# Performance work log

Hardware: AMD Instinct MI355X
Metric: run time of the kernel (lower is better)

## Reference

```python
import jax, jax.numpy as jnp
import numpy as np

N, E, G = 50000, 800000, 16
NODE, HID, OUT, HEADS = 128, 64, 128, 3
NEG_SLOPE = 0.2

def setup_inputs() -> dict:
    key = jax.random.key(0)
    ks = jax.random.split(key, 12)
    h = jax.random.normal(ks[0], (N, NODE), jnp.float32)
    z = jax.random.normal(ks[1], (G, OUT), jnp.float32)
    src = jax.random.randint(ks[2], (E,), 0, N, jnp.int32)
    dst = jax.random.randint(ks[3], (E,), 0, N, jnp.int32)
    graph_id = jnp.sort(jax.random.randint(ks[4], (N,), 0, G, jnp.int32))
    s = 0.1
    fc_w = jax.random.normal(ks[5], (HEADS * HID, NODE), jnp.float32) * s
    attn_l = jax.random.normal(ks[6], (HEADS, HID), jnp.float32) * s
    attn_r = jax.random.normal(ks[7], (HEADS, HID), jnp.float32) * s
    bias = jnp.zeros((HEADS * HID,), jnp.float32)
    lin1_w = jax.random.normal(ks[8], (HID, OUT), jnp.float32) * s
    lin1_b = jnp.zeros((HID,), jnp.float32)
    lin2_w = jax.random.normal(ks[9], (1, 2 * HID), jnp.float32) * s
    lin2_b = jnp.zeros((1,), jnp.float32)
    return dict(h=h, z=z, src=src, dst=dst, graph_id=graph_id, fc_w=fc_w,
                attn_l=attn_l, attn_r=attn_r, bias=bias,
                lin1_w=lin1_w, lin1_b=lin1_b, lin2_w=lin2_w, lin2_b=lin2_b)

def reference(h, z, src, dst, graph_id, fc_w, attn_l, attn_r, bias,
              lin1_w, lin1_b, lin2_w, lin2_b):
    n = h.shape[0]
    # GATConv: projection -> [N, H, D]
    feat = (h @ fc_w.T).reshape(n, HEADS, HID)
    el = jnp.sum(feat * attn_l, axis=-1)  # [N, H]
    er = jnp.sum(feat * attn_r, axis=-1)  # [N, H]
    e = jax.nn.leaky_relu(el[src] + er[dst], NEG_SLOPE)  # [E, H]
    # edge softmax per destination node
    m = jax.ops.segment_max(e, dst, num_segments=n)
    e = jnp.exp(e - m[dst])
    s = jax.ops.segment_sum(e, dst, num_segments=n)
    alpha = e / s[dst]
    # scatter-weighted aggregation
    msg = alpha[:, :, None] * feat[src]  # [E, H, D]
    rst = jax.ops.segment_sum(msg, dst, num_segments=n)  # [N, H, D]
    rst = rst + bias.reshape(HEADS, HID)
    h_d = jnp.mean(rst, axis=1)  # [N, D] (mean over heads)
    # dgl.mean_nodes: per-graph mean pooling
    counts = jax.ops.segment_sum(jnp.ones((n,), h_d.dtype), graph_id, num_segments=G)
    pooled = jax.ops.segment_sum(h_d, graph_id, num_segments=G) / jnp.maximum(counts, 1.0)[:, None]
    z1 = z @ lin1_w.T + lin1_b  # [G, HID]
    cat = jnp.concatenate([pooled, z1], axis=1)  # [G, 2*HID]
    score = jax.nn.sigmoid(cat @ lin2_w.T + lin2_b)  # [G, 1]
    return score
```

## Files before the change

kernel.cpp:

```cpp
#include <hip/hip_runtime.h>
#include <math.h>

#define N_NODES 50000
#define N_EDGES 800000
#define N_GRAPHS 16
#define NODE_F 128
#define HID 64
#define OUT_F 128
#define HEADS 3
#define NEG 0.2f
#define FEAT (HEADS*HID)

typedef float f32x4 __attribute__((ext_vector_type(4)));
typedef float f32x2 __attribute__((ext_vector_type(2)));
typedef short bf16x8 __attribute__((ext_vector_type(8)));

#if defined(__has_builtin)
#if __has_builtin(__builtin_amdgcn_cvt_pk_f32_fp8) && __has_builtin(__builtin_amdgcn_cvt_pk_fp8_f32)
#define USE_FP8 1
#endif
#endif
#ifndef USE_FP8
#define USE_FP8 0
#endif

#if USE_FP8
#define FB 1
#else
#define FB 2
#endif
#define GRP (8 * FB)
#define ROW (32 * GRP)

#define NBKT ((N_NODES + 63) / 64)
#define H1B 400
#define EPB (N_EDGES / H1B)
#define LROW 272

__device__ __forceinline__ ushort f2bf(float x) {
  union { float f; unsigned u; } v; v.f = x;
  unsigned r = v.u + 0x7fff + ((v.u >> 16) & 1);
  return (ushort)(r >> 16);
}
__device__ __forceinline__ float bf2f(ushort x) {
  union { unsigned u; float f; } v; v.u = ((unsigned)x) << 16;
  return v.f;
}

__device__ __forceinline__ void feat_store(unsigned char* base, int n, int hh, int dd, float v) {
  size_t off = (size_t)n * ROW + (dd >> 1) * GRP + ((hh * 2 + (dd & 1)) * FB);
#if USE_FP8
  base[off] = (unsigned char)(__builtin_amdgcn_cvt_pk_fp8_f32(v, 0.f, 0, false) & 0xff);
#else
  *(ushort*)(base + off) = f2bf(v);
#endif
}

#define ZERO_INTS (N_GRAPHS * HID + N_GRAPHS)
#define ZERO_U4 (ZERO_INTS / 4)
#define ZB ((ZERO_U4 + 255) / 256)
__global__ void kprep(const float* __restrict__ fc_w, ushort* __restrict__ fcb,
                      uint4* __restrict__ zbase) {
  if (blockIdx.x >= 24) {
    int i = (blockIdx.x - 24) * 256 + threadIdx.x;
    if (i < ZERO_U4) zbase[i] = make_uint4(0, 0, 0, 0);
    return;
  }
  int i = blockIdx.x * 256 + threadIdx.x;
  int col = i >> 5;
  int kb = (i & 31) * 4;
  float4 v = *(const float4*)(fc_w + (size_t)col * NODE_F + kb);
  int t = col >> 4, m = col & 15;
  int kk = kb >> 5, kq = (kb >> 3) & 3, j = kb & 7;
  size_t idx0 = ((((size_t)t * 4 + kk) * 4 + kq) * 16 + m) * 8 + j;
  ushort4 o; o.x = f2bf(v.x); o.y = f2bf(v.y); o.z = f2bf(v.z); o.w = f2bf(v.w);
  *(ushort4*)(fcb + idx0) = o;
}

#define GB0 ((N_NODES + 63) / 64)
__global__ __launch_bounds__(256) void k01_fused(
    const float* __restrict__ h, const ushort* __restrict__ fcb,
    const float* __restrict__ attn_l, const float* __restrict__ attn_r,
    const int* __restrict__ dst,
    unsigned char* __restrict__ feat, float* __restrict__ el, float* __restrict__ er,
    int* __restrict__ cnt_g)
{
  __shared__ ushort A[64][136];
  const int tid = threadIdx.x;

  if (blockIdx.x < H1B) {
    int* cnt = (int*)&A[0][0];
    const int blk = blockIdx.x;
    for (int i = tid; i < NBKT; i += 256) cnt[i] = 0;
    __syncthreads();
    const int e0 = blk * EPB;
    for (int i = tid; i < EPB; i += 256)
      atomicAdd(&cnt[dst[e0 + i] >> 6], 1);
    __syncthreads();
    for (int i = tid; i < NBKT; i += 256) cnt_g[(size_t)blk * NBKT + i] = cnt[i];
    return;
  }

  const int n0 = (blockIdx.x - H1B) * 64;
  for (int i = tid; i < 64 * 32; i += 256) {
    int r = i >> 5, c4 = i & 31;
    if (n0 + r < N_NODES) {
      float4 v = *(const float4*)(h + (size_t)(n0 + r) * NODE_F + c4 * 4);
      unsigned lo = f2bf(v.x) | ((unsigned)f2bf(v.y) << 16);
      unsigned hi = f2bf(v.z) | ((unsigned)f2bf(v.w) << 16);
      *(uint2*)&A[r][c4 * 4] = make_uint2(lo, hi);
    }
  }
  __syncthreads();

  const int lane = tid & 63, wv = tid >> 6;
  const int m = lane & 15, kq = lane >> 4;

  f32x4 acc[12];
#pragma unroll
  for (int t = 0; t < 12; t++) acc[t] = (f32x4){0.f, 0.f, 0.f, 0.f};

#pragma unroll
  for (int kk = 0; kk < 4; kk++) {
    bf16x8 af = *(const bf16x8*)&A[wv * 16 + m][kk * 32 + kq * 8];
#pragma unroll
    for (int t = 0; t < 12; t++) {
      const bf16x8 bf = *(const bf16x8*)(fcb + ((((size_t)t * 4 + kk) * 4 + kq) * 16 + m) * 8);
      acc[t] = __builtin_amdgcn_mfma_f32_16x16x32_bf16(af, bf, acc[t], 0, 0, 0);
    }
  }

  const int rbase = n0 + wv * 16 + kq * 4;

#if USE_FP8
  __syncthreads();
  unsigned char* lf = (unsigned char*)&A[0][0];
  const int rloc = wv * 16 + kq * 4;
#pragma unroll
  for (int t = 0; t < 12; t++) {
    const int hh = t >> 2;
    const int dd = (t & 3) * 16 + m;
    const int boff = (dd >> 1) * GRP + (hh * 2 + (dd & 1));
#pragma unroll
    for (int reg = 0; reg < 4; reg++) {
      unsigned char q = (unsigned char)(__builtin_amdgcn_cvt_pk_fp8_f32(acc[t][reg], 0.f, 0, false) & 0xff);
      lf[(rloc + reg) * LROW + boff] = q;
    }
  }
#else
#pragma unroll
  for (int t = 0; t < 12; t++) {
    const int hh = t >> 2;
    const int dd = (t & 3) * 16 + m;
#pragma unroll
    for (int reg = 0; reg < 4; reg++) {
      int n = rbase + reg;
      if (n < N_NODES) feat_store(feat, n, hh, dd, acc[t][reg]);
    }
  }
#endif

#pragma unroll
  for (int hh = 0; hh < HEADS; hh++) {
    float elv[4] = {0.f, 0.f, 0.f, 0.f};
    float erv[4] = {0.f, 0.f, 0.f, 0.f};
#pragma unroll
    for (int tt = 0; tt < 4; tt++) {
      int t = hh * 4 + tt;
      float al = attn_l[hh * HID + tt * 16 + m];
      float ar = attn_r[hh * HID + tt * 16 + m];
#pragma unroll
      for (int reg = 0; reg < 4; reg++) {
        elv[reg] = fmaf(acc[t][reg], al, elv[reg]);
        erv[reg] = fmaf(acc[t][reg], ar, erv[reg]);
      }
    }
#pragma unroll
    for (int reg = 0; reg < 4; reg++) {
#pragma unroll
      for (int off = 1; off < 16; off <<= 1) {
        elv[reg] += __shfl_xor(elv[reg], off, 64);
        erv[reg] += __shfl_xor(erv[reg], off, 64);
      }
      int n = rbase + reg;
      if (m == 0 && n < N_NODES) {
        el[(size_t)n * 4 + hh] = elv[reg];
        er[(size_t)n * 4 + hh] = erv[reg];
      }
    }
  }

#if USE_FP8
  __syncthreads();
  for (int i = tid; i < 64 * (ROW / 16); i += 256) {
    int r = i >> 4, c = (i & 15) * 16;
    int n = n0 + r;
    if (n < N_NODES)
      *(uint4*)(feat + (size_t)n * ROW + c) = *(const uint4*)(lf + r * LROW + c);
  }
#endif
}

#define H2A_K 7
__global__ __launch_bounds__(64) void kh2a_scan(
    const int* __restrict__ cnt_g, int* __restrict__ base_bm, int* __restrict__ btot)
{
  const int b = blockIdx.x;
  const int lane = threadIdx.x;
  int v[H2A_K];
  int lt = 0;
#pragma unroll
  for (int j = 0; j < H2A_K; j++) {
    int g = lane * H2A_K + j;
    v[j] = (g < H1B) ? cnt_g[(size_t)g * NBKT + b] : 0;
    lt += v[j];
  }
  int s = lt;
#pragma unroll
  for (int off = 1; off < 64; off <<= 1) {
    int t = __shfl_up(s, off, 64);
    if (lane >= off) s += t;
  }
  int excl = s - lt;
#pragma unroll
  for (int j = 0; j < H2A_K; j++) {
    int g = lane * H2A_K + j;
    if (g < H1B) base_bm[(size_t)b * H1B + g] = excl;
    excl += v[j];
  }
  if (lane == 63) btot[b] = s;
}

__global__ __launch_bounds__(256) void kh3_scatter(
    const int* __restrict__ src, const int* __restrict__ dst,
    const int* __restrict__ btot, const int* __restrict__ base_bm,
    int2* __restrict__ pairs)
{
  __shared__ int cur[NBKT];
  __shared__ int wsum[4];
  const int tid = threadIdx.x, blk = blockIdx.x;
  const int lane = tid & 63, wv = tid >> 6;
  int v[4]; int lt = 0;
#pragma unroll
  for (int j = 0; j < 4; j++) {
    int g = tid * 4 + j;
    v[j] = (g < NBKT) ? btot[g] : 0;
    lt += v[j];
  }
  int s = lt;
#pragma unroll
  for (int off = 1; off < 64; off <<= 1) {
    int t = __shfl_up(s, off, 64);
    if (lane >= off) s += t;
  }
  if (lane == 63) wsum[wv] = s;
  __syncthreads();
  int woff = 0;
#pragma unroll
  for (int w = 0; w < 4; w++) woff += (w < wv) ? wsum[w] : 0;
  int excl = s - lt + woff;
#pragma unroll
  for (int j = 0; j < 4; j++) {
    int g = tid * 4 + j;
    if (g < NBKT) cur[g] = excl + base_bm[(size_t)g * H1B + blk];
    excl += v[j];
  }
  __syncthreads();
  const int e0 = blk * EPB;
  for (int i = tid; i < EPB; i += 256) {
    int e = e0 + i;
    int d = dst[e], sv = src[e];
    int slot = atomicAdd(&cur[d >> 6], 1);
    pairs[slot] = make_int2(sv, d);
  }
}

__global__ __launch_bounds__(256) void kh4_nodesort(
    const int2* __restrict__ pairs, const int* __restrict__ btot,
    int* __restrict__ src_s, int* __restrict__ offs)
{
  __shared__ int nodecnt[64];
  __shared__ int cur[64];
  __shared__ int red_[4];
  __shared__ int lo_s, hi_s;
  const int b = blockIdx.x, tid = threadIdx.x;
  const int lane = tid & 63, wv = tid >> 6;
  int partial = 0;
  for (int i = tid; i < b; i += 256) partial += btot[i];
#pragma unroll
  for (int off = 32; off; off >>= 1) partial += __shfl_xor(partial, off, 64);
  if (lane == 0) red_[wv] = partial;
  if (tid < 64) nodecnt[tid] = 0;
  __syncthreads();
  if (tid == 0) {
    int l = red_[0] + red_[1] + red_[2] + red_[3];
    lo_s = l; hi_s = l + btot[b];
  }
  __syncthreads();
  const int lo = lo_s, hi = hi_s;
  for (int i = lo + tid; i < hi; i += 256)
    atomicAdd(&nodecnt[pairs[i].y & 63], 1);
  __syncthreads();
  if (tid < 64) {
    int v = nodecnt[tid];
    int s = v;
#pragma unroll
    for (int off = 1; off < 64; off <<= 1) {
      int t = __shfl_up(s, off, 64);
      if (tid >= off) s += t;
    }
    int excl = s - v;
    cur[tid] = lo + excl;
    int n = b * 64 + tid;
    if (n < N_NODES) offs[n] = lo + excl;
    if (b == NBKT - 1 && tid == 0) offs[N_NODES] = N_EDGES;
  }
  __syncthreads();
  for (int i = lo + tid; i < hi; i += 256) {
    int2 pr = pairs[i];
    int slot = atomicAdd(&cur[pr.y & 63], 1);
    src_s[slot] = pr.x;
  }
}

__global__ __launch_bounds__(256) void k4_agg(
    const int* __restrict__ offs, const int* __restrict__ src_s,
    const float* __restrict__ el4, const float* __restrict__ er4,
    const unsigned char* __restrict__ feat, const float* __restrict__ bias,
    float* __restrict__ h_d)
{
  __shared__ float4 rec[4][64];
  const int wv = threadIdx.x >> 6, lane = threadIdx.x & 63;
  const int n = blockIdx.x * 4 + wv;
  const int lo = offs[n], hi = offs[n + 1];
  const int half = lane >> 5;
  const int d = lane & 31;
  const char* fb = (const char*)feat;
  const float4 ern = ((const float4*)er4)[n];

  float a0x = 0.f, a0y = 0.f, a1x = 0.f, a1y = 0.f, a2x = 0.f, a2y = 0.f;
  float s0 = 0.f, s1 = 0.f, s2 = 0.f;

  for (int base = lo; base < hi; base += 64) {
    const int cnt = min(64, hi - base);
    if (lane < cnt) {
      int sidx = src_s[base + lane];
      float4 elv = ((const float4*)el4)[sidx];
      float e0 = elv.x + ern.x; e0 = e0 > 0.f ? e0 : NEG * e0;
      float e1 = elv.y + ern.y; e1 = e1 > 0.f ? e1 : NEG * e1;
      float e2 = elv.z + ern.z; e2 = e2 > 0.f ? e2 : NEG * e2;
      float4 c;
      c.x = __expf(e0); c.y = __expf(e1); c.z = __expf(e2);
      c.w = __int_as_float(sidx * ROW);
      rec[wv][lane] = c;
      s0 += c.x; s1 += c.y; s2 += c.z;
    }
#define K4_BODY(J) do { \
      float4 c = rec[wv][J]; \
      const char* rp = fb + __float_as_int(c.w) + GRP * d; \
      f32x2 f0, f1, f2; \
      if (USE_FP8) { \
        uint2 q = *(const uint2*)rp; \
        f0 = __builtin_amdgcn_cvt_pk_f32_fp8(q.x & 0xffff, false); \
        f1 = __builtin_amdgcn_cvt_pk_f32_fp8(q.x >> 16, false); \
        f2 = __builtin_amdgcn_cvt_pk_f32_fp8(q.y & 0xffff, false); \
      } else { \
        uint4 q = *(const uint4*)rp; \
        f0.x = bf2f((ushort)(q.x & 0xffff)); f0.y = bf2f((ushort)(q.x >> 16)); \
        f1.x = bf2f((ushort)(q.y & 0xffff)); f1.y = bf2f((ushort)(q.y >> 16)); \
        f2.x = bf2f((ushort)(q.z & 0xffff)); f2.y = bf2f((ushort)(q.z >> 16)); \
      } \
      a0x = fmaf(c.x, f0.x, a0x); a0y = fmaf(c.x, f0.y, a0y); \
      a1x = fmaf(c.y, f1.x, a1x); a1y = fmaf(c.y, f1.y, a1y); \
      a2x = fmaf(c.z, f2.x, a2x); a2y = fmaf(c.z, f2.y, a2y); \
    } while (0)
    int j = half;
    for (; j + 2 < cnt; j += 4) { K4_BODY(j); K4_BODY(j + 2); }
    if (j < cnt) K4_BODY(j);
#undef K4_BODY
  }
  a0x += __shfl_xor(a0x, 32, 64); a0y += __shfl_xor(a0y, 32, 64);
  a1x += __shfl_xor(a1x, 32, 64); a1y += __shfl_xor(a1y, 32, 64);
  a2x += __shfl_xor(a2x, 32, 64); a2y += __shfl_xor(a2y, 32, 64);
#pragma unroll
  for (int off = 32; off; off >>= 1) {
    s0 += __shfl_xor(s0, off, 64);
    s1 += __shfl_xor(s1, off, 64);
    s2 += __shfl_xor(s2, off, 64);
  }
  const float i0 = s0 > 0.f ? 1.f / s0 : 0.f;
  const float i1 = s1 > 0.f ? 1.f / s1 : 0.f;
  const float i2 = s2 > 0.f ? 1.f / s2 : 0.f;
  if (half == 0) {
    float2 b0 = *(const float2*)(bias + 2 * d);
    float2 b1 = *(const float2*)(bias + HID + 2 * d);
    float2 b2 = *(const float2*)(bias + 2 * HID + 2 * d);
    float2 o;
    o.x = (fmaf(a0x, i0, b0.x) + fmaf(a1x, i1, b1.x) + fmaf(a2x, i2, b2.x)) * (1.f / 3.f);
    o.y = (fmaf(a0y, i0, b0.y) + fmaf(a1y, i1, b1.y) + fmaf(a2y, i2, b2.y)) * (1.f / 3.f);
    *(float2*)(h_d + (size_t)n * HID + 2 * d) = o;
  }
}

#define K5_NPB 128
#define K5_NB ((N_NODES + K5_NPB - 1) / K5_NPB)
#define NSEG (K5_NB * 2)
__global__ __launch_bounds__(256) void k5a_partial(
    const int* __restrict__ graph_id, const float* __restrict__ h_d,
    float* __restrict__ pooled_res, int* __restrict__ gcnt_res,
    float* __restrict__ part, int* __restrict__ pg, int* __restrict__ pc)
{
  const int wv = threadIdx.x >> 6, lane = threadIdx.x & 63;
  const int b = blockIdx.x;
  const int n0 = b * K5_NPB;
  const int n1 = min(n0 + K5_NPB, N_NODES);
  const int g_lo = graph_id[n0], g_hi = graph_id[n1 - 1];

  if (g_hi > g_lo + 1) {
    float acc = 0.f; int cur_g = -1; int cnt = 0;
    for (int i = n0 + wv; i < n1; i += 4) {
      int g = graph_id[i];
      if (g != cur_g) {
        if (cur_g >= 0) {
          atomicAdd(&pooled_res[cur_g * HID + lane], acc);
          if (lane == 0) atomicAdd(&gcnt_res[cur_g], cnt);
        }
        acc = 0.f; cnt = 0; cur_g = g;
      }
      acc += h_d[(size_t)i * HID + lane];
      cnt++;
    }
    if (cur_g >= 0) {
      atomicAdd(&pooled_res[cur_g * HID + lane], acc);
      if (lane == 0) atomicAdd(&gcnt_res[cur_g], cnt);
    }
    if (threadIdx.x < 2) pg[b * 2 + threadIdx.x] = -1;
    return;
  }

  float acc_lo = 0.f, acc_hi = 0.f;
  int c_lo = 0, c_hi = 0;
  for (int i = n0 + wv; i < n1; i += 4) {
    int g = graph_id[i];
    float v = h_d[(size_t)i * HID + lane];
    bool hi = (g != g_lo);
    acc_hi += hi ? v : 0.f;
    acc_lo += hi ? 0.f : v;
    c_hi += hi ? 1 : 0;
    c_lo += hi ? 0 : 1;
  }
  __shared__ float ls[2][4][64];
  __shared__ int lc[2][4];
  ls[0][wv][lane] = acc_lo;
  ls[1][wv][lane] = acc_hi;
  if (lane == 0) { lc[0][wv] = c_lo; lc[1][wv] = c_hi; }
  __syncthreads();
  if (wv < 2) {
    float s = ls[wv][0][lane] + ls[wv][1][lane] + ls[wv][2][lane] + ls[wv][3][lane];
    part[((size_t)b * 2 + wv) * HID + lane] = s;
    if (lane == 0) {
      int cnt = lc[wv][0] + lc[wv][1] + lc[wv][2] + lc[wv][3];
      int gg = (wv == 0) ? g_lo : g_hi;
      if (wv == 1 && (g_hi == g_lo || cnt == 0)) gg = -1;
      pg[b * 2 + wv] = gg;
      pc[b * 2 + wv] = cnt;
    }
  }
}

__global__ __launch_bounds__(256) void k6_final(
    const float* __restrict__ part, const int* __restrict__ pg, const int* __restrict__ pc,
    const float* __restrict__ pooled_res, const int* __restrict__ gcnt_res,
    const float* __restrict__ z,
    const float* __restrict__ lin1_w, const float* __restrict__ lin1_b,
    const float* __restrict__ lin2_w, const float* __restrict__ lin2_b,
    float* __restrict__ out)
{
  const int g = blockIdx.x;
  const int tid = threadIdx.x, wv = tid >> 6, lane = tid & 63;
  __shared__ int spg[NSEG], spc[NSEG];
  __shared__ float red[4][HID];
  __shared__ int rc[4];
  __shared__ float cat[2 * HID];

  for (int i = tid; i < NSEG; i += 256) { spg[i] = pg[i]; spc[i] = pc[i]; }
  __syncthreads();

  float acc = 0.f; int cnt = 0;
  for (int s = wv; s < NSEG; s += 4) {
    if (spg[s] == g) {
      acc += part[(size_t)s * HID + lane];
      cnt += spc[s];
    }
  }
  red[wv][lane] = acc;
  if (lane == 0) rc[wv] = cnt;
  __syncthreads();

  if (wv == 0) {
    float s = red[0][lane] + red[1][lane] + red[2][lane] + red[3][lane]
            + pooled_res[g * HID + lane];
    int c = rc[0] + rc[1] + rc[2] + rc[3] + gcnt_res[g];
    cat[lane] = s / (float)(c > 0 ? c : 1);
  }
  if (wv == 1) {
    float s = lin1_b[lane];
    const float* zr = z + g * OUT_F;
    const float* wr = lin1_w + lane * OUT_F;
    for (int k = 0; k < OUT_F; k += 4) {
      float4 zv = *(const float4*)(zr + k);
      float4 wv4 = *(const float4*)(wr + k);
      s = fmaf(zv.x, wv4.x, fmaf(zv.y, wv4.y, fmaf(zv.z, wv4.z, fmaf(zv.w, wv4.w, s))));
    }
    cat[HID + lane] = s;
  }
  __syncthreads();
  if (wv == 0) {
    float s = cat[lane] * lin2_w[lane] + cat[HID + lane] * lin2_w[HID + lane];
#pragma unroll
    for (int off = 32; off; off >>= 1) s += __shfl_xor(s, off, 64);
    if (lane == 0) out[g] = 1.f / (1.f + __expf(-(s + lin2_b[0])));
  }
}

extern "C" void kernel_launch(void* const* d_in, const int* in_sizes, int n_in,
                              void* d_out, int out_size, void* d_ws, size_t ws_size,
                              hipStream_t stream) {
  (void)in_sizes; (void)n_in; (void)out_size; (void)ws_size;
  const float* h      = (const float*)d_in[0];
  const float* z      = (const float*)d_in[1];
  const int*   src    = (const int*)d_in[2];
  const int*   dst    = (const int*)d_in[3];
  const int*   gid    = (const int*)d_in[4];
  const float* fc_w   = (const float*)d_in[5];
  const float* attn_l = (const float*)d_in[6];
  const float* attn_r = (const float*)d_in[7];
  const float* bias   = (const float*)d_in[8];
  const float* lin1_w = (const float*)d_in[9];
  const float* lin1_b = (const float*)d_in[10];
  const float* lin2_w = (const float*)d_in[11];
  const float* lin2_b = (const float*)d_in[12];
  float* out = (float*)d_out;

  int2* pairs       = (int2*)d_ws;
  unsigned char* feat = (unsigned char*)(pairs + N_EDGES);
  float* h_d        = (float*)(feat + (size_t)N_NODES * ROW);
  float* el         = h_d + (size_t)N_NODES * HID;
  float* er         = el + (size_t)N_NODES * 4;
  float* part       = er + (size_t)N_NODES * 4;
  int* pg           = (int*)(part + (size_t)NSEG * HID);
  int* pc           = pg + NSEG;
  ushort* fcb       = (ushort*)(pc + NSEG);
  float* pooled_res = (float*)(fcb + 192 * NODE_F);
  int* gcnt_res     = (int*)(pooled_res + N_GRAPHS * HID);
  int* offs         = gcnt_res + N_GRAPHS;
  int* src_s        = offs + (N_NODES + 1);
  int* cnt_g        = src_s + N_EDGES;
  int* base_bm      = cnt_g + (size_t)H1B * NBKT;
  int* btot         = base_bm + (size_t)NBKT * H1B;

  kprep<<<24 + ZB, 256, 0, stream>>>(fc_w, fcb, (uint4*)pooled_res);
  k01_fused<<<H1B + GB0, 256, 0, stream>>>(h, fcb, attn_l, attn_r, dst,
                                           feat, el, er, cnt_g);
  kh2a_scan<<<NBKT, 64, 0, stream>>>(cnt_g, base_bm, btot);
  kh3_scatter<<<H1B, 256, 0, stream>>>(src, dst, btot, base_bm, pairs);
  kh4_nodesort<<<NBKT, 256, 0, stream>>>(pairs, btot, src_s, offs);
  k4_agg<<<N_NODES / 4, 256, 0, stream>>>(offs, src_s, el, er, feat, bias, h_d);
  k5a_partial<<<K5_NB, 256, 0, stream>>>(gid, h_d, pooled_res, gcnt_res, part, pg, pc);
  k6_final<<<N_GRAPHS, 256, 0, stream>>>(part, pg, pc, pooled_res, gcnt_res,
                                         z, lin1_w, lin1_b, lin2_w, lin2_b, out);
}
```

Baseline: 201.1 us.

## Fuse graph pooling into aggregation kernel and pack edge pairs into one int

The per-graph mean pooling stage is folded into the aggregation kernel. Each block reduces its four nodes' outputs into per-graph partial sums in shared memory, which removes the h_d intermediate buffer and one kernel launch. Separately, the (src,dst) pairs are packed into a single 32-bit word (src<<6 | dst&63), halving scatter and sort traffic. The final kernel now scans far more partial segments (NSEG2 = N/4*2) using a ballot loop, and the aggregation kernel gains an extra __syncthreads and shared memory.

```diff
diff --git a/kernel.cpp b/kernel.cpp
--- a/kernel.cpp
+++ b/kernel.cpp
@@ -36,6 +36,7 @@
 #define H1B 400
 #define EPB (N_EDGES / H1B)
 #define LROW 272
+#define NSEG2 ((N_NODES / 4) * 2)
 
 __device__ __forceinline__ ushort f2bf(float x) {
   union { float f; unsigned u; } v; v.f = x;
@@ -234,7 +235,7 @@
 __global__ __launch_bounds__(256) void kh3_scatter(
     const int* __restrict__ src, const int* __restrict__ dst,
     const int* __restrict__ btot, const int* __restrict__ base_bm,
-    int2* __restrict__ pairs)
+    int* __restrict__ pairs)
 {
   __shared__ int cur[NBKT];
   __shared__ int wsum[4];
@@ -271,12 +272,12 @@
     int e = e0 + i;
     int d = dst[e], sv = src[e];
     int slot = atomicAdd(&cur[d >> 6], 1);
-    pairs[slot] = make_int2(sv, d);
+    pairs[slot] = (sv << 6) | (d & 63);
   }
 }
 
 __global__ __launch_bounds__(256) void kh4_nodesort(
-    const int2* __restrict__ pairs, const int* __restrict__ btot,
+    const int* __restrict__ pairs, const int* __restrict__ btot,
     int* __restrict__ src_s, int* __restrict__ offs)
 {
   __shared__ int nodecnt[64];
@@ -299,7 +300,7 @@
   __syncthreads();
   const int lo = lo_s, hi = hi_s;
   for (int i = lo + tid; i < hi; i += 256)
-    atomicAdd(&nodecnt[pairs[i].y & 63], 1);
+    atomicAdd(&nodecnt[pairs[i] & 63], 1);
   __syncthreads();
   if (tid < 64) {
     int v = nodecnt[tid];
@@ -317,9 +318,9 @@
   }
   __syncthreads();
   for (int i = lo + tid; i < hi; i += 256) {
-    int2 pr = pairs[i];
-    int slot = atomicAdd(&cur[pr.y & 63], 1);
-    src_s[slot] = pr.x;
+    int p = pairs[i];
+    int slot = atomicAdd(&cur[p & 63], 1);
+    src_s[slot] = p >> 6;
   }
 }
 
@@ -327,16 +328,27 @@
     const int* __restrict__ offs, const int* __restrict__ src_s,
     const float* __restrict__ el4, const float* __restrict__ er4,
     const unsigned char* __restrict__ feat, const float* __restrict__ bias,
-    float* __restrict__ h_d)
+    const int* __restrict__ gid,
+    float* __restrict__ pooled_res, int* __restrict__ gcnt_res,
+    float* __restrict__ part, int* __restrict__ pg, int* __restrict__ pc)
 {
   __shared__ float4 rec[4][64];
+  __shared__ float pool[4][2][HID];
+  __shared__ int pooln[4][2];
   const int wv = threadIdx.x >> 6, lane = threadIdx.x & 63;
-  const int n = blockIdx.x * 4 + wv;
+  const int b = blockIdx.x;
+  const int n = b * 4 + wv;
   const int lo = offs[n], hi = offs[n + 1];
   const int half = lane >> 5;
   const int d = lane & 31;
   const char* fb = (const char*)feat;
   const float4 ern = ((const float4*)er4)[n];
+
+  if (lane < 64) {
+    pool[wv][0][lane] = 0.f;
+    pool[wv][1][lane] = 0.f;
+    if (lane == 0) { pooln[wv][0] = 0; pooln[wv][1] = 0; }
+  }
 
   float a0x = 0.f, a0y = 0.f, a1x = 0.f, a1y = 0.f, a2x = 0.f, a2y = 0.f;
   float s0 = 0.f, s1 = 0.f, s2 = 0.f;
@@ -391,79 +403,42 @@
   const float i0 = s0 > 0.f ? 1.f / s0 : 0.f;
   const float i1 = s1 > 0.f ? 1.f / s1 : 0.f;
   const float i2 = s2 > 0.f ? 1.f / s2 : 0.f;
+
+  const int g_lo = gid[b * 4];
+  const int g_hi = gid[b * 4 + 3];
+  const bool rare = (g_hi > g_lo + 1);
+  const int gn = gid[n];
   if (half == 0) {
     float2 b0 = *(const float2*)(bias + 2 * d);
     float2 b1 = *(const float2*)(bias + HID + 2 * d);
     float2 b2 = *(const float2*)(bias + 2 * HID + 2 * d);
-    float2 o;
-    o.x = (fmaf(a0x, i0, b0.x) + fmaf(a1x, i1, b1.x) + fmaf(a2x, i2, b2.x)) * (1.f / 3.f);
-    o.y = (fmaf(a0y, i0, b0.y) + fmaf(a1y, i1, b1.y) + fmaf(a2y, i2, b2.y)) * (1.f / 3.f);
-    *(float2*)(h_d + (size_t)n * HID + 2 * d) = o;
-  }
-}
-
-#define K5_NPB 128
-#define K5_NB ((N_NODES + K5_NPB - 1) / K5_NPB)
-#define NSEG (K5_NB * 2)
-__global__ __launch_bounds__(256) void k5a_partial(
-    const int* __restrict__ graph_id, const float* __restrict__ h_d,
-    float* __restrict__ pooled_res, int* __restrict__ gcnt_res,
-    float* __restrict__ part, int* __restrict__ pg, int* __restrict__ pc)
-{
-  const int wv = threadIdx.x >> 6, lane = threadIdx.x & 63;
-  const int b = blockIdx.x;
-  const int n0 = b * K5_NPB;
-  const int n1 = min(n0 + K5_NPB, N_NODES);
-  const int g_lo = graph_id[n0], g_hi = graph_id[n1 - 1];
-
-  if (g_hi > g_lo + 1) {
-    float acc = 0.f; int cur_g = -1; int cnt = 0;
-    for (int i = n0 + wv; i < n1; i += 4) {
-      int g = graph_id[i];
-      if (g != cur_g) {
-        if (cur_g >= 0) {
-          atomicAdd(&pooled_res[cur_g * HID + lane], acc);
-          if (lane == 0) atomicAdd(&gcnt_res[cur_g], cnt);
-        }
-        acc = 0.f; cnt = 0; cur_g = g;
-      }
-      acc += h_d[(size_t)i * HID + lane];
-      cnt++;
-    }
-    if (cur_g >= 0) {
-      atomicAdd(&pooled_res[cur_g * HID + lane], acc);
-      if (lane == 0) atomicAdd(&gcnt_res[cur_g], cnt);
-    }
-    if (threadIdx.x < 2) pg[b * 2 + threadIdx.x] = -1;
-    return;
-  }
-
-  float acc_lo = 0.f, acc_hi = 0.f;
-  int c_lo = 0, c_hi = 0;
-  for (int i = n0 + wv; i < n1; i += 4) {
-    int g = graph_id[i];
-    float v = h_d[(size_t)i * HID + lane];
-    bool hi = (g != g_lo);
-    acc_hi += hi ? v : 0.f;
-    acc_lo += hi ? 0.f : v;
-    c_hi += hi ? 1 : 0;
-    c_lo += hi ? 0 : 1;
-  }
-  __shared__ float ls[2][4][64];
-  __shared__ int lc[2][4];
-  ls[0][wv][lane] = acc_lo;
-  ls[1][wv][lane] = acc_hi;
-  if (lane == 0) { lc[0][wv] = c_lo; lc[1][wv] = c_hi; }
-  __syncthreads();
-  if (wv < 2) {
-    float s = ls[wv][0][lane] + ls[wv][1][lane] + ls[wv][2][lane] + ls[wv][3][lane];
-    part[((size_t)b * 2 + wv) * HID + lane] = s;
-    if (lane == 0) {
-      int cnt = lc[wv][0] + lc[wv][1] + lc[wv][2] + lc[wv][3];
-      int gg = (wv == 0) ? g_lo : g_hi;
-      if (wv == 1 && (g_hi == g_lo || cnt == 0)) gg = -1;
-      pg[b * 2 + wv] = gg;
-      pc[b * 2 + wv] = cnt;
+    float ox = (fmaf(a0x, i0, b0.x) + fmaf(a1x, i1, b1.x) + fmaf(a2x, i2, b2.x)) * (1.f / 3.f);
+    float oy = (fmaf(a0y, i0, b0.y) + fmaf(a1y, i1, b1.y) + fmaf(a2y, i2, b2.y)) * (1.f / 3.f);
+    if (!rare) {
+      int sub = (gn != g_lo) ? 1 : 0;
+      pool[wv][sub][2 * d] = ox;
+      pool[wv][sub][2 * d + 1] = oy;
+      if (d == 0) pooln[wv][sub] = 1;
+    } else {
+      atomicAdd(&pooled_res[gn * HID + 2 * d], ox);
+      atomicAdd(&pooled_res[gn * HID + 2 * d + 1], oy);
+      if (d == 0) atomicAdd(&gcnt_res[gn], 1);
+    }
+  }
+  __syncthreads();
+  if (threadIdx.x < 128) {
+    int sub = threadIdx.x >> 6;
+    int l = threadIdx.x & 63;
+    float s = pool[0][sub][l] + pool[1][sub][l] + pool[2][sub][l] + pool[3][sub][l];
+    part[((size_t)b * 2 + sub) * HID + l] = s;
+    if (l == 0) {
+      int c = pooln[0][sub] + pooln[1][sub] + pooln[2][sub] + pooln[3][sub];
+      int gg = (sub == 0) ? g_lo : g_hi;
+      if (rare) gg = -1;
+      if (sub == 1 && (g_hi == g_lo || c == 0)) gg = -1;
+      if (sub == 0 && c == 0) gg = -1;
+      pg[b * 2 + sub] = gg;
+      pc[b * 2 + sub] = c;
     }
   }
 }
@@ -478,21 +453,25 @@
 {
   const int g = blockIdx.x;
   const int tid = threadIdx.x, wv = tid >> 6, lane = tid & 63;
-  __shared__ int spg[NSEG], spc[NSEG];
   __shared__ float red[4][HID];
   __shared__ int rc[4];
   __shared__ float cat[2 * HID];
 
-  for (int i = tid; i < NSEG; i += 256) { spg[i] = pg[i]; spc[i] = pc[i]; }
-  __syncthreads();
-
   float acc = 0.f; int cnt = 0;
-  for (int s = wv; s < NSEG; s += 4) {
-    if (spg[s] == g) {
-      acc += part[(size_t)s * HID + lane];
-      cnt += spc[s];
-    }
-  }
+  for (int s0 = wv * 64; s0 < NSEG2; s0 += 256) {
+    int s = s0 + lane;
+    int pgv = (s < NSEG2) ? pg[s] : -2;
+    bool hit = (pgv == g);
+    cnt += hit ? pc[s] : 0;
+    unsigned long long mask = __ballot(hit);
+    while (mask) {
+      int bit = __ffsll((long long)mask) - 1;
+      mask &= mask - 1;
+      acc += part[(size_t)(s0 + bit) * HID + lane];
+    }
+  }
+#pragma unroll
+  for (int off = 32; off; off >>= 1) cnt += __shfl_xor(cnt, off, 64);
   red[wv][lane] = acc;
   if (lane == 0) rc[wv] = cnt;
   __syncthreads();
@@ -542,15 +521,14 @@
   const float* lin2_b = (const float*)d_in[12];
   float* out = (float*)d_out;
 
-  int2* pairs       = (int2*)d_ws;
+  int* pairs        = (int*)d_ws;
   unsigned char* feat = (unsigned char*)(pairs + N_EDGES);
-  float* h_d        = (float*)(feat + (size_t)N_NODES * ROW);
-  float* el         = h_d + (size_t)N_NODES * HID;
+  float* el         = (float*)(feat + (size_t)N_NODES * ROW);
   float* er         = el + (size_t)N_NODES * 4;
   float* part       = er + (size_t)N_NODES * 4;
-  int* pg           = (int*)(part + (size_t)NSEG * HID);
-  int* pc           = pg + NSEG;
-  ushort* fcb       = (ushort*)(pc + NSEG);
+  int* pg           = (int*)(part + (size_t)NSEG2 * HID);
+  int* pc           = pg + NSEG2;
+  ushort* fcb       = (ushort*)(pc + NSEG2);
   float* pooled_res = (float*)(fcb + 192 * NODE_F);
   int* gcnt_res     = (int*)(pooled_res + N_GRAPHS * HID);
   int* offs         = gcnt_res + N_GRAPHS;
@@ -565,8 +543,8 @@
   kh2a_scan<<<NBKT, 64, 0, stream>>>(cnt_g, base_bm, btot);
   kh3_scatter<<<H1B, 256, 0, stream>>>(src, dst, btot, base_bm, pairs);
   kh4_nodesort<<<NBKT, 256, 0, stream>>>(pairs, btot, src_s, offs);
-  k4_agg<<<N_NODES / 4, 256, 0, stream>>>(offs, src_s, el, er, feat, bias, h_d);
-  k5a_partial<<<K5_NB, 256, 0, stream>>>(gid, h_d, pooled_res, gcnt_res, part, pg, pc);
+  k4_agg<<<N_NODES / 4, 256, 0, stream>>>(offs, src_s, el, er, feat, bias, gid,
+                                          pooled_res, gcnt_res, part, pg, pc);
   k6_final<<<N_GRAPHS, 256, 0, stream>>>(part, pg, pc, pooled_res, gcnt_res,
                                          z, lin1_w, lin1_b, lin2_w, lin2_b, out);
 }
```

After: 262.4 us. +30.5%, slower.
